# Kernel optimization log

Hardware: AMD Instinct MI355X
Metric: run time of the kernel (lower is better)

## Reference

```python
import jax, jax.numpy as jnp
import numpy as np

B, N, CIN = 4, 8192, 256
H, D = 8, 64            # n_heads, head_n_channels
INNER = H * D           # 512
COUT = 256
EPS = 1e-5              # torch InstanceNorm1d default eps


def setup_inputs() -> dict:
    key = jax.random.key(0)
    ks = jax.random.split(key, 8)
    s = 1.0 / np.sqrt(CIN)
    return {
        "u_x": jax.random.normal(ks[0], (B, N, CIN), dtype=jnp.float32),
        "pos_x": jax.random.uniform(ks[1], (B, N, 2), dtype=jnp.float32),
        # torch nn.Linear weights have shape (out_features, in_features)
        "Wq": jax.random.normal(ks[2], (INNER, CIN), dtype=jnp.float32) * s,
        "Wk": jax.random.normal(ks[3], (INNER, CIN), dtype=jnp.float32) * s,
        "Wv": jax.random.normal(ks[4], (INNER, CIN), dtype=jnp.float32) * s,
        "Wo": jax.random.normal(ks[5], (COUT, INNER), dtype=jnp.float32) * (1.0 / np.sqrt(INNER)),
        "bo": jax.random.normal(ks[6], (COUT,), dtype=jnp.float32) * 0.01,
    }


def _heads(x, W):
    # x: [B,N,CIN] @ W.T -> [B,N,H*D] -> [B,H,N,D]
    y = jnp.einsum("bnc,ec->bne", x, W)
    return y.reshape(x.shape[0], x.shape[1], H, D).transpose(0, 2, 1, 3)


def _inorm(u):
    # Matches torch: InstanceNorm1d applied to (B*H, N, D) normalizes over the
    # LAST dim (D) per (batch, head, grid point), biased variance, no affine.
    mean = jnp.mean(u, axis=-1, keepdims=True)
    var = jnp.mean(jnp.square(u - mean), axis=-1, keepdims=True)
    return (u - mean) / jnp.sqrt(var + EPS)


def reference(u_x, pos_x, Wq, Wk, Wv, Wo, bo):
    batch, n = u_x.shape[0], u_x.shape[1]
    q = _heads(u_x, Wq)          # [B,H,N,D]
    k = _inorm(_heads(u_x, Wk))  # u_y = u_x (self-attention path)
    v = _inorm(_heads(u_x, Wv))
    # associative path: (K^T V) then Q; uniform weights = 1/N
    dots = jnp.einsum("bhnd,bhne->bhde", k, v)   # [B,H,D,D]
    u = jnp.einsum("bhnd,bhde->bhne", q, dots) / n
    u = u.transpose(0, 2, 1, 3).reshape(batch, n, INNER)
    return jnp.einsum("bne,oe->bno", u, Wo) + bo
```

## Files before the change

kernel.cpp:

```cpp
#include <hip/hip_runtime.h>


#define B_    4
#define N_    8192
#define CIN_  256
#define H_    8
#define D_    64
#define INNER_ 512
#define COUT_ 256
#define EPS_  1e-5f

typedef unsigned short ushort_t;
typedef unsigned int   uint_t;
typedef __attribute__((ext_vector_type(8))) short short8;
typedef __attribute__((ext_vector_type(4))) float f32x4;

__device__ __forceinline__ void split_bf16(float x, ushort_t& hi, ushort_t& lo) {
  const uint_t u = __float_as_uint(x);
  const uint_t hr = (u + 0x8000u) & 0xffff0000u;
  hi = (ushort_t)(hr >> 16);
  const float l = x - __uint_as_float(hr);
  lo = (ushort_t)((__float_as_uint(l) + 0x8000u) >> 16);
}

__device__ __forceinline__ void cvt8(float4 x, float4 y, uint4& uh, uint4& ul) {
  const float v[8] = {x.x, x.y, x.z, x.w, y.x, y.y, y.z, y.w};
  ushort_t h[8], l[8];
#pragma unroll
  for (int j = 0; j < 8; j++) split_bf16(v[j], h[j], l[j]);
  uh = make_uint4(h[0] | ((uint_t)h[1] << 16), h[2] | ((uint_t)h[3] << 16),
                  h[4] | ((uint_t)h[5] << 16), h[6] | ((uint_t)h[7] << 16));
  ul = make_uint4(l[0] | ((uint_t)l[1] << 16), l[2] | ((uint_t)l[3] << 16),
                  l[4] | ((uint_t)l[5] << 16), l[6] | ((uint_t)l[7] << 16));
}

#define MFMA(A, Bv, C) __builtin_amdgcn_mfma_f32_16x16x32_bf16((A), (Bv), (C), 0, 0, 0)

__global__ __launch_bounds__(256) void prep_ux_kernel(
    const float* __restrict__ u_x, ushort_t* __restrict__ uxH,
    ushort_t* __restrict__ uxL)
{
  const size_t base = ((size_t)blockIdx.x * 256 + threadIdx.x) * 8;
  const float4 x = *(const float4*)(u_x + base);
  const float4 y = *(const float4*)(u_x + base + 4);
  uint4 uh, ul;
  cvt8(x, y, uh, ul);
  *(uint4*)(uxH + base) = uh;
  *(uint4*)(uxL + base) = ul;
}

__global__ __launch_bounds__(256) void prep_w_kernel(
    const float* __restrict__ Wk, const float* __restrict__ Wv,
    ushort_t* __restrict__ WkvH, ushort_t* __restrict__ WkvL)
{
  const size_t base = ((size_t)blockIdx.x * 256 + threadIdx.x) * 8;
  const float* src = (base < 131072) ? (Wk + base) : (Wv + base - 131072);
  const float4 x = *(const float4*)(src);
  const float4 y = *(const float4*)(src + 4);
  uint4 uh, ul;
  cvt8(x, y, uh, ul);
  *(uint4*)(WkvH + base) = uh;
  *(uint4*)(WkvL + base) = ul;
}

__global__ __launch_bounds__(256, 2) void kv_dots_kernel(
    const ushort_t* __restrict__ uxH, const ushort_t* __restrict__ uxL,
    const ushort_t* __restrict__ WkvH, const ushort_t* __restrict__ WkvL,
    float* __restrict__ dots)
{
  __shared__ __align__(16) char smem[36864];
  ushort_t (*Ah)[130][8] = (ushort_t(*)[130][8])(smem);
  ushort_t (*Al)[130][8] = (ushort_t(*)[130][8])(smem + 8320);
  ushort_t (*Bh)[130][8] = (ushort_t(*)[130][8])(smem + 16640);
  ushort_t (*Bl)[130][8] = (ushort_t(*)[130][8])(smem + 24960);
  ushort_t* KtH = (ushort_t*)(smem);
  ushort_t* KtL = (ushort_t*)(smem + 9216);
  ushort_t* VtH = (ushort_t*)(smem + 18432);
  ushort_t* VtL = (ushort_t*)(smem + 27648);

  const int t = threadIdx.x;
  const int chunk = blockIdx.x, h = blockIdx.y, b = blockIdx.z;
  const int lane = t & 63, wave = t >> 6;
  const int q = lane >> 4, r = lane & 15;
  const int m0 = (wave >> 1) * 64, n0 = (wave & 1) * 64;
  const int srow = t >> 1, scs = (t & 1) * 16, q0 = (t & 1) * 2;
  const int dstripe = 16 * wave;

  const int wr = (srow < 64) ? (h * 64 + srow) : (512 + h * 64 + srow - 64);
  const ushort_t* bgH = WkvH + (size_t)wr * CIN_ + scs;
  const ushort_t* bgL = WkvL + (size_t)wr * CIN_ + scs;

  f32x4 dacc[4];
#pragma unroll
  for (int j = 0; j < 4; j++) dacc[j] = (f32x4)0.f;

  for (int mt = 0; mt < 2; mt++) {
    const int r0 = chunk * 256 + mt * 128;
    const ushort_t* agH = uxH + ((size_t)(b * N_) + r0 + srow) * CIN_ + scs;
    const ushort_t* agL = uxL + ((size_t)(b * N_) + r0 + srow) * CIN_ + scs;

    f32x4 acc[4][4];
#pragma unroll
    for (int i = 0; i < 4; i++)
#pragma unroll
      for (int j = 0; j < 4; j++) acc[i][j] = (f32x4)0.f;

    for (int kc = 0; kc < 8; kc++) {
      *(uint4*)&Ah[q0][srow][0]     = *(const uint4*)(agH + kc * 32);
      *(uint4*)&Ah[q0 + 1][srow][0] = *(const uint4*)(agH + kc * 32 + 8);
      *(uint4*)&Al[q0][srow][0]     = *(const uint4*)(agL + kc * 32);
      *(uint4*)&Al[q0 + 1][srow][0] = *(const uint4*)(agL + kc * 32 + 8);
      *(uint4*)&Bh[q0][srow][0]     = *(const uint4*)(bgH + kc * 32);
      *(uint4*)&Bh[q0 + 1][srow][0] = *(const uint4*)(bgH + kc * 32 + 8);
      *(uint4*)&Bl[q0][srow][0]     = *(const uint4*)(bgL + kc * 32);
      *(uint4*)&Bl[q0 + 1][srow][0] = *(const uint4*)(bgL + kc * 32 + 8);
      __syncthreads();
      short8 ahf[4], alf[4];
#pragma unroll
      for (int mi = 0; mi < 4; mi++) {
        ahf[mi] = *(const short8*)&Ah[q][m0 + 16 * mi + r][0];
        alf[mi] = *(const short8*)&Al[q][m0 + 16 * mi + r][0];
      }
#pragma unroll
      for (int nj = 0; nj < 4; nj++) {
        const short8 bhv = *(const short8*)&Bh[q][n0 + 16 * nj + r][0];
        const short8 blv = *(const short8*)&Bl[q][n0 + 16 * nj + r][0];
#pragma unroll
        for (int mi = 0; mi < 4; mi++) {
          acc[mi][nj] = MFMA(ahf[mi], bhv, acc[mi][nj]);
          acc[mi][nj] = MFMA(alf[mi], bhv, acc[mi][nj]);
          acc[mi][nj] = MFMA(ahf[mi], blv, acc[mi][nj]);
        }
      }
      __syncthreads();
    }

    float mean[4][4], inv[4][4];
#pragma unroll
    for (int mi = 0; mi < 4; mi++)
#pragma unroll
      for (int reg = 0; reg < 4; reg++) {
        float rs = 0.f, rq = 0.f;
#pragma unroll
        for (int nj = 0; nj < 4; nj++) {
          const float v = acc[mi][nj][reg];
          rs += v;
          rq = fmaf(v, v, rq);
        }
#pragma unroll
        for (int msk = 1; msk < 16; msk <<= 1) {
          rs += __shfl_xor(rs, msk, 64);
          rq += __shfl_xor(rq, msk, 64);
        }
        const float m = rs * (1.f / 64.f);
        const float var = fmaxf(rq * (1.f / 64.f) - m * m, 0.f);
        mean[mi][reg] = m;
        inv[mi][reg] = rsqrtf(var + EPS_);
      }
#pragma unroll
    for (int mi = 0; mi < 4; mi++)
#pragma unroll
      for (int nj = 0; nj < 4; nj++)
#pragma unroll
        for (int reg = 0; reg < 4; reg++)
          acc[mi][nj][reg] = (acc[mi][nj][reg] - mean[mi][reg]) * inv[mi][reg];

    for (int p = 0; p < 2; p++) {
      if ((wave >> 1) == p) {
        ushort_t* Hd = (wave & 1) ? VtH : KtH;
        ushort_t* Ld = (wave & 1) ? VtL : KtL;
#pragma unroll
        for (int nj = 0; nj < 4; nj++) {
          const int d = 16 * nj + r;
#pragma unroll
          for (int mi = 0; mi < 4; mi++) {
            const int nb = 16 * mi + 4 * q;
            ushort_t hh[4], ll[4];
#pragma unroll
            for (int reg = 0; reg < 4; reg++)
              split_bf16(acc[mi][nj][reg], hh[reg], ll[reg]);
            uint2 ph, pl;
            ph.x = hh[0] | ((uint_t)hh[1] << 16);
            ph.y = hh[2] | ((uint_t)hh[3] << 16);
            pl.x = ll[0] | ((uint_t)ll[1] << 16);
            pl.y = ll[2] | ((uint_t)ll[3] << 16);
            *(uint2*)&Hd[d * 72 + nb] = ph;
            *(uint2*)&Ld[d * 72 + nb] = pl;
          }
        }
      }
      __syncthreads();
#pragma unroll
      for (int ks = 0; ks < 2; ks++) {
        const short8 aH = *(const short8*)&KtH[(dstripe + r) * 72 + ks * 32 + q * 8];
        const short8 aL = *(const short8*)&KtL[(dstripe + r) * 72 + ks * 32 + q * 8];
#pragma unroll
        for (int ej = 0; ej < 4; ej++) {
          const short8 bH = *(const short8*)&VtH[(16 * ej + r) * 72 + ks * 32 + q * 8];
          const short8 bL = *(const short8*)&VtL[(16 * ej + r) * 72 + ks * 32 + q * 8];
          dacc[ej] = MFMA(aH, bH, dacc[ej]);
          dacc[ej] = MFMA(aL, bH, dacc[ej]);
          dacc[ej] = MFMA(aH, bL, dacc[ej]);
        }
      }
      __syncthreads();
    }
  }

  float* dg = dots + ((size_t)(b * H_ + h)) * 4096;
#pragma unroll
  for (int ej = 0; ej < 4; ej++)
#pragma unroll
    for (int reg = 0; reg < 4; reg++)
      atomicAdd(&dg[(dstripe + 4 * q + reg) * 64 + 16 * ej + r], dacc[ej][reg]);
}

__global__ __launch_bounds__(256) void s_kernel(
    const float* __restrict__ dots, const float* __restrict__ Wo,
    float* __restrict__ S)
{
  const int blk = blockIdx.x;
  const int b = blk >> 9, hd = blk & 511, h = hd >> 6;
  __shared__ float drow[64];
  const int t = threadIdx.x;
  if (t < 64) drow[t] = dots[((size_t)(b * H_ + h)) * 4096 + (hd & 63) * 64 + t];
  __syncthreads();
  const float* wp = Wo + (size_t)t * INNER_ + h * 64;
  float acc = 0.f;
#pragma unroll
  for (int e = 0; e < 64; e += 4) {
    const float4 w = *(const float4*)(wp + e);
    acc = fmaf(drow[e + 0], w.x, acc);
    acc = fmaf(drow[e + 1], w.y, acc);
    acc = fmaf(drow[e + 2], w.z, acc);
    acc = fmaf(drow[e + 3], w.w, acc);
  }
  S[((size_t)(b * INNER_) + hd) * COUT_ + t] = acc;
}

__global__ __launch_bounds__(256) void mb_part_kernel(
    const float* __restrict__ Wq, const float* __restrict__ S,
    float* __restrict__ Mbp)
{
  __shared__ __align__(16) float wql[128][16];
  const int c0 = blockIdx.x * 16, b = blockIdx.y, s = blockIdx.z;
  const int t = threadIdx.x;
#pragma unroll
  for (int i = 0; i < 8; i++) {
    const int idx = i * 256 + t;
    wql[idx >> 4][idx & 15] = Wq[(size_t)(s * 128 + (idx >> 4)) * CIN_ + c0 + (idx & 15)];
  }
  __syncthreads();
  float acc[16];
#pragma unroll
  for (int cp = 0; cp < 16; cp++) acc[cp] = 0.f;
  const float* sp = S + ((size_t)(b * INNER_) + s * 128) * COUT_ + t;
  for (int hd = 0; hd < 128; hd++) {
    const float sv = sp[(size_t)hd * COUT_];
#pragma unroll
    for (int g = 0; g < 4; g++) {
      const float4 w = *(const float4*)&wql[hd][g * 4];
      acc[g * 4 + 0] = fmaf(w.x, sv, acc[g * 4 + 0]);
      acc[g * 4 + 1] = fmaf(w.y, sv, acc[g * 4 + 1]);
      acc[g * 4 + 2] = fmaf(w.z, sv, acc[g * 4 + 2]);
      acc[g * 4 + 3] = fmaf(w.w, sv, acc[g * 4 + 3]);
    }
  }
#pragma unroll
  for (int cp = 0; cp < 16; cp++)
    Mbp[(((size_t)s * 4 + b) * CIN_ + c0 + cp) * COUT_ + t] = acc[cp];
}

__global__ __launch_bounds__(256) void mb_merge_kernel(
    const float* __restrict__ Mbp, ushort_t* __restrict__ MbtH,
    ushort_t* __restrict__ MbtL)
{
  const int c0 = blockIdx.x * 16, b = blockIdx.y;
  const int o = threadIdx.x;
#pragma unroll
  for (int cp = 0; cp < 16; cp++) {
    const int c = c0 + cp;
    float v = 0.f;
#pragma unroll
    for (int s = 0; s < 4; s++)
      v += Mbp[(((size_t)s * 4 + b) * CIN_ + c) * COUT_ + o];
    v *= (1.0f / N_);
    ushort_t hi, lo;
    split_bf16(v, hi, lo);
    const size_t off = ((size_t)(b * COUT_) + o) * CIN_ + c;
    MbtH[off] = hi;
    MbtL[off] = lo;
  }
}

__global__ __launch_bounds__(256, 2) void out_kernel(
    const ushort_t* __restrict__ uxH, const ushort_t* __restrict__ uxL,
    const ushort_t* __restrict__ MbtH, const ushort_t* __restrict__ MbtL,
    const float* __restrict__ bo, float* __restrict__ out)
{
  __shared__ __align__(16) char smem[33280];
  ushort_t (*Ah)[130][8] = (ushort_t(*)[130][8])(smem);
  ushort_t (*Al)[130][8] = (ushort_t(*)[130][8])(smem + 8320);
  ushort_t (*Bh)[130][8] = (ushort_t(*)[130][8])(smem + 16640);
  ushort_t (*Bl)[130][8] = (ushort_t(*)[130][8])(smem + 24960);

  const int t = threadIdx.x;
  const int r0 = blockIdx.x * 128, o0 = blockIdx.y * 128, b = blockIdx.z;
  const int lane = t & 63, wave = t >> 6;
  const int q = lane >> 4, r = lane & 15;
  const int m0 = (wave >> 1) * 64, n0 = (wave & 1) * 64;
  const int srow = t >> 1, scs = (t & 1) * 16, q0 = (t & 1) * 2;

  const ushort_t* agH = uxH + ((size_t)(b * N_) + r0 + srow) * CIN_ + scs;
  const ushort_t* agL = uxL + ((size_t)(b * N_) + r0 + srow) * CIN_ + scs;
  const ushort_t* bgH = MbtH + ((size_t)(b * COUT_) + o0 + srow) * CIN_ + scs;
  const ushort_t* bgL = MbtL + ((size_t)(b * COUT_) + o0 + srow) * CIN_ + scs;

  f32x4 acc[4][4];
#pragma unroll
  for (int i = 0; i < 4; i++)
#pragma unroll
    for (int j = 0; j < 4; j++) acc[i][j] = (f32x4)0.f;

  for (int kc = 0; kc < 8; kc++) {
    *(uint4*)&Ah[q0][srow][0]     = *(const uint4*)(agH + kc * 32);
    *(uint4*)&Ah[q0 + 1][srow][0] = *(const uint4*)(agH + kc * 32 + 8);
    *(uint4*)&Al[q0][srow][0]     = *(const uint4*)(agL + kc * 32);
    *(uint4*)&Al[q0 + 1][srow][0] = *(const uint4*)(agL + kc * 32 + 8);
    *(uint4*)&Bh[q0][srow][0]     = *(const uint4*)(bgH + kc * 32);
    *(uint4*)&Bh[q0 + 1][srow][0] = *(const uint4*)(bgH + kc * 32 + 8);
    *(uint4*)&Bl[q0][srow][0]     = *(const uint4*)(bgL + kc * 32);
    *(uint4*)&Bl[q0 + 1][srow][0] = *(const uint4*)(bgL + kc * 32 + 8);
    __syncthreads();
    short8 ahf[4], alf[4];
#pragma unroll
    for (int mi = 0; mi < 4; mi++) {
      ahf[mi] = *(const short8*)&Ah[q][m0 + 16 * mi + r][0];
      alf[mi] = *(const short8*)&Al[q][m0 + 16 * mi + r][0];
    }
#pragma unroll
    for (int nj = 0; nj < 4; nj++) {
      const short8 bhv = *(const short8*)&Bh[q][n0 + 16 * nj + r][0];
      const short8 blv = *(const short8*)&Bl[q][n0 + 16 * nj + r][0];
#pragma unroll
      for (int mi = 0; mi < 4; mi++) {
        acc[mi][nj] = MFMA(ahf[mi], bhv, acc[mi][nj]);
        acc[mi][nj] = MFMA(alf[mi], bhv, acc[mi][nj]);
        acc[mi][nj] = MFMA(ahf[mi], blv, acc[mi][nj]);
      }
    }
    __syncthreads();
  }

  float bov[4];
#pragma unroll
  for (int nj = 0; nj < 4; nj++) bov[nj] = bo[o0 + n0 + 16 * nj + r];
#pragma unroll
  for (int mi = 0; mi < 4; mi++)
#pragma unroll
    for (int nj = 0; nj < 4; nj++) {
      const f32x4 v = acc[mi][nj];
#pragma unroll
      for (int reg = 0; reg < 4; reg++) {
        const int row = r0 + m0 + 16 * mi + q * 4 + reg;
        out[((size_t)(b * N_) + row) * COUT_ + o0 + n0 + 16 * nj + r] =
            v[reg] + bov[nj];
      }
    }
}

extern "C" void kernel_launch(void* const* d_in, const int* in_sizes, int n_in,
                              void* d_out, int out_size, void* d_ws, size_t ws_size,
                              hipStream_t stream) {
  const float* u_x = (const float*)d_in[0];
  const float* Wq = (const float*)d_in[2];
  const float* Wk = (const float*)d_in[3];
  const float* Wv = (const float*)d_in[4];
  const float* Wo = (const float*)d_in[5];
  const float* bo = (const float*)d_in[6];
  float* out = (float*)d_out;

  ushort_t* uxH  = (ushort_t*)d_ws;
  ushort_t* uxL  = uxH + 8388608;
  ushort_t* WkvH = uxL + 8388608;
  ushort_t* WkvL = WkvH + 262144;
  ushort_t* MbtH = WkvL + 262144;
  ushort_t* MbtL = MbtH + 262144;
  float* dots = (float*)(MbtL + 262144);
  float* S    = dots + 131072;
  float* Mbp  = S + 524288;

  prep_ux_kernel<<<4096, 256, 0, stream>>>(u_x, uxH, uxL);
  prep_w_kernel<<<128, 256, 0, stream>>>(Wk, Wv, WkvH, WkvL);
  hipMemsetAsync(dots, 0, 131072 * sizeof(float), stream);
  kv_dots_kernel<<<dim3(32, 8, 4), 256, 0, stream>>>(uxH, uxL, WkvH, WkvL, dots);
  s_kernel<<<2048, 256, 0, stream>>>(dots, Wo, S);
  mb_part_kernel<<<dim3(16, 4, 4), 256, 0, stream>>>(Wq, S, Mbp);
  mb_merge_kernel<<<dim3(16, 4), 256, 0, stream>>>(Mbp, MbtH, MbtL);
  out_kernel<<<dim3(64, 2, 4), 256, 0, stream>>>(uxH, uxL, MbtH, MbtL, bo, out);
}
```

Measured before the change: 232.3 us.

## Stage GEMM tiles with direct global-to-LDS loads in kv_dots and out kernels

Replaces register-staged global→LDS copies in the kv_dots and out GEMM loops with __builtin_amdgcn_global_load_lds 16-byte direct transfers. Each wave now owns one operand plane (A hi, A lo, B hi, B lo) and loads 64 rows per instruction into an unpadded LDS layout. This removes the VGPR round trip and ds_write instructions, but drops the 130-row padding, which may add LDS bank conflicts on fragment reads. There is no visible wait for the async loads before __syncthreads, so correctness depends on the compiler inserting vmcnt waits.

```diff
diff --git a/kernel.cpp b/kernel.cpp
--- a/kernel.cpp
+++ b/kernel.cpp
@@ -36,6 +36,12 @@
 
 #define MFMA(A, Bv, C) __builtin_amdgcn_mfma_f32_16x16x32_bf16((A), (Bv), (C), 0, 0, 0)
 
+__device__ __forceinline__ void gload_lds16(const ushort_t* g, char* l) {
+  __builtin_amdgcn_global_load_lds(
+      (const __attribute__((address_space(1))) void*)(const void*)g,
+      (__attribute__((address_space(3))) void*)(void*)l, 16, 0, 0);
+}
+
 __global__ __launch_bounds__(256) void prep_ux_kernel(
     const float* __restrict__ u_x, ushort_t* __restrict__ uxH,
     ushort_t* __restrict__ uxL)
@@ -69,10 +75,10 @@
     float* __restrict__ dots)
 {
   __shared__ __align__(16) char smem[36864];
-  ushort_t (*Ah)[130][8] = (ushort_t(*)[130][8])(smem);
-  ushort_t (*Al)[130][8] = (ushort_t(*)[130][8])(smem + 8320);
-  ushort_t (*Bh)[130][8] = (ushort_t(*)[130][8])(smem + 16640);
-  ushort_t (*Bl)[130][8] = (ushort_t(*)[130][8])(smem + 24960);
+  ushort_t (*Ah)[128][8] = (ushort_t(*)[128][8])(smem);
+  ushort_t (*Al)[128][8] = (ushort_t(*)[128][8])(smem + 8192);
+  ushort_t (*Bh)[128][8] = (ushort_t(*)[128][8])(smem + 16384);
+  ushort_t (*Bl)[128][8] = (ushort_t(*)[128][8])(smem + 24576);
   ushort_t* KtH = (ushort_t*)(smem);
   ushort_t* KtL = (ushort_t*)(smem + 9216);
   ushort_t* VtH = (ushort_t*)(smem + 18432);
@@ -83,12 +89,11 @@
   const int lane = t & 63, wave = t >> 6;
   const int q = lane >> 4, r = lane & 15;
   const int m0 = (wave >> 1) * 64, n0 = (wave & 1) * 64;
-  const int srow = t >> 1, scs = (t & 1) * 16, q0 = (t & 1) * 2;
   const int dstripe = 16 * wave;
 
-  const int wr = (srow < 64) ? (h * 64 + srow) : (512 + h * 64 + srow - 64);
-  const ushort_t* bgH = WkvH + (size_t)wr * CIN_ + scs;
-  const ushort_t* bgL = WkvL + (size_t)wr * CIN_ + scs;
+  const size_t halfoff = (wave < 2) ? (size_t)(64 * CIN_) : (size_t)(512 * CIN_);
+  char* lbase = smem + wave * 8192;
+  const ushort_t* gB = ((wave == 3) ? WkvL : WkvH) + (size_t)(h * 64 + lane) * CIN_;
 
   f32x4 dacc[4];
 #pragma unroll
@@ -96,8 +101,10 @@
 
   for (int mt = 0; mt < 2; mt++) {
     const int r0 = chunk * 256 + mt * 128;
-    const ushort_t* agH = uxH + ((size_t)(b * N_) + r0 + srow) * CIN_ + scs;
-    const ushort_t* agL = uxL + ((size_t)(b * N_) + r0 + srow) * CIN_ + scs;
+    const ushort_t* gsrc =
+        (wave == 0) ? (uxH + ((size_t)(b * N_) + r0 + lane) * CIN_)
+      : (wave == 1) ? (uxL + ((size_t)(b * N_) + r0 + lane) * CIN_)
+      : gB;
 
     f32x4 acc[4][4];
 #pragma unroll
@@ -106,14 +113,11 @@
       for (int j = 0; j < 4; j++) acc[i][j] = (f32x4)0.f;
 
     for (int kc = 0; kc < 8; kc++) {
-      *(uint4*)&Ah[q0][srow][0]     = *(const uint4*)(agH + kc * 32);
-      *(uint4*)&Ah[q0 + 1][srow][0] = *(const uint4*)(agH + kc * 32 + 8);
-      *(uint4*)&Al[q0][srow][0]     = *(const uint4*)(agL + kc * 32);
-      *(uint4*)&Al[q0 + 1][srow][0] = *(const uint4*)(agL + kc * 32 + 8);
-      *(uint4*)&Bh[q0][srow][0]     = *(const uint4*)(bgH + kc * 32);
-      *(uint4*)&Bh[q0 + 1][srow][0] = *(const uint4*)(bgH + kc * 32 + 8);
-      *(uint4*)&Bl[q0][srow][0]     = *(const uint4*)(bgL + kc * 32);
-      *(uint4*)&Bl[q0 + 1][srow][0] = *(const uint4*)(bgL + kc * 32 + 8);
+      const ushort_t* gk = gsrc + kc * 32;
+#pragma unroll
+      for (int j = 0; j < 8; j++)
+        gload_lds16(gk + (size_t)(j & 1) * halfoff + (j >> 1) * 8,
+                    lbase + j * 1024);
       __syncthreads();
       short8 ahf[4], alf[4];
 #pragma unroll
@@ -298,23 +302,25 @@
     const ushort_t* __restrict__ MbtH, const ushort_t* __restrict__ MbtL,
     const float* __restrict__ bo, float* __restrict__ out)
 {
-  __shared__ __align__(16) char smem[33280];
-  ushort_t (*Ah)[130][8] = (ushort_t(*)[130][8])(smem);
-  ushort_t (*Al)[130][8] = (ushort_t(*)[130][8])(smem + 8320);
-  ushort_t (*Bh)[130][8] = (ushort_t(*)[130][8])(smem + 16640);
-  ushort_t (*Bl)[130][8] = (ushort_t(*)[130][8])(smem + 24960);
+  __shared__ __align__(16) char smem[32768];
+  ushort_t (*Ah)[128][8] = (ushort_t(*)[128][8])(smem);
+  ushort_t (*Al)[128][8] = (ushort_t(*)[128][8])(smem + 8192);
+  ushort_t (*Bh)[128][8] = (ushort_t(*)[128][8])(smem + 16384);
+  ushort_t (*Bl)[128][8] = (ushort_t(*)[128][8])(smem + 24576);
 
   const int t = threadIdx.x;
   const int r0 = blockIdx.x * 128, o0 = blockIdx.y * 128, b = blockIdx.z;
   const int lane = t & 63, wave = t >> 6;
   const int q = lane >> 4, r = lane & 15;
   const int m0 = (wave >> 1) * 64, n0 = (wave & 1) * 64;
-  const int srow = t >> 1, scs = (t & 1) * 16, q0 = (t & 1) * 2;
-
-  const ushort_t* agH = uxH + ((size_t)(b * N_) + r0 + srow) * CIN_ + scs;
-  const ushort_t* agL = uxL + ((size_t)(b * N_) + r0 + srow) * CIN_ + scs;
-  const ushort_t* bgH = MbtH + ((size_t)(b * COUT_) + o0 + srow) * CIN_ + scs;
-  const ushort_t* bgL = MbtL + ((size_t)(b * COUT_) + o0 + srow) * CIN_ + scs;
+
+  char* lbase = smem + wave * 8192;
+  const size_t halfoff = (size_t)(64 * CIN_);
+  const ushort_t* gsrc =
+      (wave == 0) ? (uxH + ((size_t)(b * N_) + r0 + lane) * CIN_)
+    : (wave == 1) ? (uxL + ((size_t)(b * N_) + r0 + lane) * CIN_)
+    : (wave == 2) ? (MbtH + ((size_t)(b * COUT_) + o0 + lane) * CIN_)
+    :               (MbtL + ((size_t)(b * COUT_) + o0 + lane) * CIN_);
 
   f32x4 acc[4][4];
 #pragma unroll
@@ -323,14 +329,11 @@
     for (int j = 0; j < 4; j++) acc[i][j] = (f32x4)0.f;
 
   for (int kc = 0; kc < 8; kc++) {
-    *(uint4*)&Ah[q0][srow][0]     = *(const uint4*)(agH + kc * 32);
-    *(uint4*)&Ah[q0 + 1][srow][0] = *(const uint4*)(agH + kc * 32 + 8);
-    *(uint4*)&Al[q0][srow][0]     = *(const uint4*)(agL + kc * 32);
-    *(uint4*)&Al[q0 + 1][srow][0] = *(const uint4*)(agL + kc * 32 + 8);
-    *(uint4*)&Bh[q0][srow][0]     = *(const uint4*)(bgH + kc * 32);
-    *(uint4*)&Bh[q0 + 1][srow][0] = *(const uint4*)(bgH + kc * 32 + 8);
-    *(uint4*)&Bl[q0][srow][0]     = *(const uint4*)(bgL + kc * 32);
-    *(uint4*)&Bl[q0 + 1][srow][0] = *(const uint4*)(bgL + kc * 32 + 8);
+    const ushort_t* gk = gsrc + kc * 32;
+#pragma unroll
+    for (int j = 0; j < 8; j++)
+      gload_lds16(gk + (size_t)(j & 1) * halfoff + (j >> 1) * 8,
+                  lbase + j * 1024);
     __syncthreads();
     short8 ahf[4], alf[4];
 #pragma unroll
```

Result: slower. 315.6 us (+35.9%).

## Pre-tile operands into MFMA fragment layout and load directly from global memory

Applied to the files above, without the earlier changes.

The prep kernels and the Mb merge now write bf16 hi/lo operands in a tiled layout where each 16x32 MFMA fragment is a contiguous 64-lane x 8-element block. The kv_dots and out GEMM loops then read fragments straight from global memory with one coalesced 16-byte load per lane, removing the shared-memory staging and both __syncthreads per k-step. The cost is that every wave reloads A and B fragments from global/L2 memory instead of sharing them through LDS, which raises cache traffic. There is also no explicit prefetch across k-steps.

```diff
diff --git a/kernel.cpp b/kernel.cpp
--- a/kernel.cpp
+++ b/kernel.cpp
@@ -36,31 +36,45 @@
 
 #define MFMA(A, Bv, C) __builtin_amdgcn_mfma_f32_16x16x32_bf16((A), (Bv), (C), 0, 0, 0)
 
+
 __global__ __launch_bounds__(256) void prep_ux_kernel(
     const float* __restrict__ u_x, ushort_t* __restrict__ uxH,
     ushort_t* __restrict__ uxL)
 {
-  const size_t base = ((size_t)blockIdx.x * 256 + threadIdx.x) * 8;
+  const uint_t tid = blockIdx.x * 256 + threadIdx.x;
+  const size_t base = (size_t)tid * 8;
   const float4 x = *(const float4*)(u_x + base);
   const float4 y = *(const float4*)(u_x + base + 4);
   uint4 uh, ul;
   cvt8(x, y, uh, ul);
-  *(uint4*)(uxH + base) = uh;
-  *(uint4*)(uxL + base) = ul;
+  const uint_t g = tid >> 5;
+  const uint_t c0 = (tid & 31) * 8;
+  const uint_t b = g >> 13, n = g & 8191;
+  const uint_t nt = n >> 4, kt = c0 >> 5, qq = (c0 >> 3) & 3;
+  const uint_t lanei = (n & 15) | (qq << 4);
+  const size_t dst = ((((size_t)b * 512 + nt) * 8 + kt) * 64 + lanei) * 8;
+  *(uint4*)(uxH + dst) = uh;
+  *(uint4*)(uxL + dst) = ul;
 }
 
 __global__ __launch_bounds__(256) void prep_w_kernel(
     const float* __restrict__ Wk, const float* __restrict__ Wv,
     ushort_t* __restrict__ WkvH, ushort_t* __restrict__ WkvL)
 {
-  const size_t base = ((size_t)blockIdx.x * 256 + threadIdx.x) * 8;
-  const float* src = (base < 131072) ? (Wk + base) : (Wv + base - 131072);
+  const uint_t tid = blockIdx.x * 256 + threadIdx.x;
+  const uint_t rr = tid >> 5;
+  const uint_t c0 = (tid & 31) * 8;
+  const float* src = (rr < 512) ? (Wk + (size_t)rr * CIN_ + c0)
+                                : (Wv + (size_t)(rr - 512) * CIN_ + c0);
   const float4 x = *(const float4*)(src);
   const float4 y = *(const float4*)(src + 4);
   uint4 uh, ul;
   cvt8(x, y, uh, ul);
-  *(uint4*)(WkvH + base) = uh;
-  *(uint4*)(WkvL + base) = ul;
+  const uint_t kt = c0 >> 5, qq = (c0 >> 3) & 3;
+  const uint_t lanei = (rr & 15) | (qq << 4);
+  const size_t dst = (((size_t)(rr >> 4) * 8 + kt) * 64 + lanei) * 8;
+  *(uint4*)(WkvH + dst) = uh;
+  *(uint4*)(WkvL + dst) = ul;
 }
 
 __global__ __launch_bounds__(256, 2) void kv_dots_kernel(
@@ -69,10 +83,6 @@
     float* __restrict__ dots)
 {
   __shared__ __align__(16) char smem[36864];
-  ushort_t (*Ah)[130][8] = (ushort_t(*)[130][8])(smem);
-  ushort_t (*Al)[130][8] = (ushort_t(*)[130][8])(smem + 8320);
-  ushort_t (*Bh)[130][8] = (ushort_t(*)[130][8])(smem + 16640);
-  ushort_t (*Bl)[130][8] = (ushort_t(*)[130][8])(smem + 24960);
   ushort_t* KtH = (ushort_t*)(smem);
   ushort_t* KtL = (ushort_t*)(smem + 9216);
   ushort_t* VtH = (ushort_t*)(smem + 18432);
@@ -83,21 +93,17 @@
   const int lane = t & 63, wave = t >> 6;
   const int q = lane >> 4, r = lane & 15;
   const int m0 = (wave >> 1) * 64, n0 = (wave & 1) * 64;
-  const int srow = t >> 1, scs = (t & 1) * 16, q0 = (t & 1) * 2;
   const int dstripe = 16 * wave;
-
-  const int wr = (srow < 64) ? (h * 64 + srow) : (512 + h * 64 + srow - 64);
-  const ushort_t* bgH = WkvH + (size_t)wr * CIN_ + scs;
-  const ushort_t* bgL = WkvL + (size_t)wr * CIN_ + scs;
+  const size_t laneoff = (size_t)lane * 8;
+
+  const int rtB0 = ((wave & 1) ? 32 : 0) + h * 4;
 
   f32x4 dacc[4];
 #pragma unroll
   for (int j = 0; j < 4; j++) dacc[j] = (f32x4)0.f;
 
   for (int mt = 0; mt < 2; mt++) {
-    const int r0 = chunk * 256 + mt * 128;
-    const ushort_t* agH = uxH + ((size_t)(b * N_) + r0 + srow) * CIN_ + scs;
-    const ushort_t* agL = uxL + ((size_t)(b * N_) + r0 + srow) * CIN_ + scs;
+    const int nt0 = chunk * 16 + mt * 8 + (m0 >> 4);
 
     f32x4 acc[4][4];
 #pragma unroll
@@ -106,25 +112,19 @@
       for (int j = 0; j < 4; j++) acc[i][j] = (f32x4)0.f;
 
     for (int kc = 0; kc < 8; kc++) {
-      *(uint4*)&Ah[q0][srow][0]     = *(const uint4*)(agH + kc * 32);
-      *(uint4*)&Ah[q0 + 1][srow][0] = *(const uint4*)(agH + kc * 32 + 8);
-      *(uint4*)&Al[q0][srow][0]     = *(const uint4*)(agL + kc * 32);
-      *(uint4*)&Al[q0 + 1][srow][0] = *(const uint4*)(agL + kc * 32 + 8);
-      *(uint4*)&Bh[q0][srow][0]     = *(const uint4*)(bgH + kc * 32);
-      *(uint4*)&Bh[q0 + 1][srow][0] = *(const uint4*)(bgH + kc * 32 + 8);
-      *(uint4*)&Bl[q0][srow][0]     = *(const uint4*)(bgL + kc * 32);
-      *(uint4*)&Bl[q0 + 1][srow][0] = *(const uint4*)(bgL + kc * 32 + 8);
-      __syncthreads();
       short8 ahf[4], alf[4];
 #pragma unroll
       for (int mi = 0; mi < 4; mi++) {
-        ahf[mi] = *(const short8*)&Ah[q][m0 + 16 * mi + r][0];
-        alf[mi] = *(const short8*)&Al[q][m0 + 16 * mi + r][0];
+        const size_t toff =
+            (((size_t)b * 512 + nt0 + mi) * 8 + kc) * 512 + laneoff;
+        ahf[mi] = *(const short8*)(uxH + toff);
+        alf[mi] = *(const short8*)(uxL + toff);
       }
 #pragma unroll
       for (int nj = 0; nj < 4; nj++) {
-        const short8 bhv = *(const short8*)&Bh[q][n0 + 16 * nj + r][0];
-        const short8 blv = *(const short8*)&Bl[q][n0 + 16 * nj + r][0];
+        const size_t boff = ((size_t)(rtB0 + nj) * 8 + kc) * 512 + laneoff;
+        const short8 bhv = *(const short8*)(WkvH + boff);
+        const short8 blv = *(const short8*)(WkvL + boff);
 #pragma unroll
         for (int mi = 0; mi < 4; mi++) {
           acc[mi][nj] = MFMA(ahf[mi], bhv, acc[mi][nj]);
@@ -132,7 +132,6 @@
           acc[mi][nj] = MFMA(ahf[mi], blv, acc[mi][nj]);
         }
       }
-      __syncthreads();
     }
 
     float mean[4][4], inv[4][4];
@@ -287,7 +286,10 @@
     v *= (1.0f / N_);
     ushort_t hi, lo;
     split_bf16(v, hi, lo);
-    const size_t off = ((size_t)(b * COUT_) + o) * CIN_ + c;
+    const uint_t kt = c >> 5, qq = (c >> 3) & 3;
+    const uint_t lanei = (o & 15) | (qq << 4);
+    const size_t off =
+        ((((size_t)b * 16 + (o >> 4)) * 8 + kt) * 64 + lanei) * 8 + (c & 7);
     MbtH[off] = hi;
     MbtL[off] = lo;
   }
@@ -298,23 +300,15 @@
     const ushort_t* __restrict__ MbtH, const ushort_t* __restrict__ MbtL,
     const float* __restrict__ bo, float* __restrict__ out)
 {
-  __shared__ __align__(16) char smem[33280];
-  ushort_t (*Ah)[130][8] = (ushort_t(*)[130][8])(smem);
-  ushort_t (*Al)[130][8] = (ushort_t(*)[130][8])(smem + 8320);
-  ushort_t (*Bh)[130][8] = (ushort_t(*)[130][8])(smem + 16640);
-  ushort_t (*Bl)[130][8] = (ushort_t(*)[130][8])(smem + 24960);
-
   const int t = threadIdx.x;
   const int r0 = blockIdx.x * 128, o0 = blockIdx.y * 128, b = blockIdx.z;
   const int lane = t & 63, wave = t >> 6;
   const int q = lane >> 4, r = lane & 15;
   const int m0 = (wave >> 1) * 64, n0 = (wave & 1) * 64;
-  const int srow = t >> 1, scs = (t & 1) * 16, q0 = (t & 1) * 2;
-
-  const ushort_t* agH = uxH + ((size_t)(b * N_) + r0 + srow) * CIN_ + scs;
-  const ushort_t* agL = uxL + ((size_t)(b * N_) + r0 + srow) * CIN_ + scs;
-  const ushort_t* bgH = MbtH + ((size_t)(b * COUT_) + o0 + srow) * CIN_ + scs;
-  const ushort_t* bgL = MbtL + ((size_t)(b * COUT_) + o0 + srow) * CIN_ + scs;
+  const size_t laneoff = (size_t)lane * 8;
+
+  const int nt0 = (r0 + m0) >> 4;
+  const int ot0 = (o0 + n0) >> 4;
 
   f32x4 acc[4][4];
 #pragma unroll
@@ -323,25 +317,20 @@
     for (int j = 0; j < 4; j++) acc[i][j] = (f32x4)0.f;
 
   for (int kc = 0; kc < 8; kc++) {
-    *(uint4*)&Ah[q0][srow][0]     = *(const uint4*)(agH + kc * 32);
-    *(uint4*)&Ah[q0 + 1][srow][0] = *(const uint4*)(agH + kc * 32 + 8);
-    *(uint4*)&Al[q0][srow][0]     = *(const uint4*)(agL + kc * 32);
-    *(uint4*)&Al[q0 + 1][srow][0] = *(const uint4*)(agL + kc * 32 + 8);
-    *(uint4*)&Bh[q0][srow][0]     = *(const uint4*)(bgH + kc * 32);
-    *(uint4*)&Bh[q0 + 1][srow][0] = *(const uint4*)(bgH + kc * 32 + 8);
-    *(uint4*)&Bl[q0][srow][0]     = *(const uint4*)(bgL + kc * 32);
-    *(uint4*)&Bl[q0 + 1][srow][0] = *(const uint4*)(bgL + kc * 32 + 8);
-    __syncthreads();
     short8 ahf[4], alf[4];
 #pragma unroll
     for (int mi = 0; mi < 4; mi++) {
-      ahf[mi] = *(const short8*)&Ah[q][m0 + 16 * mi + r][0];
-      alf[mi] = *(const short8*)&Al[q][m0 + 16 * mi + r][0];
+      const size_t toff =
+          (((size_t)b * 512 + nt0 + mi) * 8 + kc) * 512 + laneoff;
+      ahf[mi] = *(const short8*)(uxH + toff);
+      alf[mi] = *(const short8*)(uxL + toff);
     }
 #pragma unroll
     for (int nj = 0; nj < 4; nj++) {
-      const short8 bhv = *(const short8*)&Bh[q][n0 + 16 * nj + r][0];
-      const short8 blv = *(const short8*)&Bl[q][n0 + 16 * nj + r][0];
+      const size_t boff =
+          (((size_t)b * 16 + ot0 + nj) * 8 + kc) * 512 + laneoff;
+      const short8 bhv = *(const short8*)(MbtH + boff);
+      const short8 blv = *(const short8*)(MbtL + boff);
 #pragma unroll
       for (int mi = 0; mi < 4; mi++) {
         acc[mi][nj] = MFMA(ahf[mi], bhv, acc[mi][nj]);
@@ -349,7 +338,6 @@
         acc[mi][nj] = MFMA(ahf[mi], blv, acc[mi][nj]);
       }
     }
-    __syncthreads();
   }
 
   float bov[4];
```

After: 235.6 us. Within noise of the previous version (+1.4%).
